# Kernel optimization log

Hardware: AMD Instinct MI355X
Metric: run time of the kernel (lower is better)

Reference implementation:

```python
import jax, jax.numpy as jnp
import numpy as np

IN_DIM = 9
HIDDEN = 32
SORT_K = 30


def setup_inputs() -> dict:
    key = jax.random.key(0)
    ks = jax.random.split(key, 16)
    N, E, G = 250000, 2500000, 2048
    x = jax.random.normal(ks[0], (N, IN_DIM), dtype=jnp.float32)
    edge_index = jax.random.randint(ks[1], (2, E), 0, N, dtype=jnp.int32)
    batch = jnp.sort(jax.random.randint(ks[2], (N,), 0, G, dtype=jnp.int32))
    s = lambda k, sh: jax.random.normal(k, sh, dtype=jnp.float32) * 0.05
    return {
        "x": x, "edge_index": edge_index, "batch": batch, "num_graphs": G,
        "W1": s(ks[3], (IN_DIM, HIDDEN)), "b1": jnp.zeros((HIDDEN,), jnp.float32),
        "W2": s(ks[4], (HIDDEN, HIDDEN)), "b2": jnp.zeros((HIDDEN,), jnp.float32),
        "W3": s(ks[5], (HIDDEN, HIDDEN)), "b3": jnp.zeros((HIDDEN,), jnp.float32),
        "cw1": s(ks[6], (16, HIDDEN, 5)), "cb1": jnp.zeros((16,), jnp.float32),
        "cw2": s(ks[7], (32, 16, 5)), "cb2": jnp.zeros((32,), jnp.float32),
        "lw1": s(ks[8], (32 * (SORT_K - 8), 128)), "lb1": jnp.zeros((128,), jnp.float32),
        "lw2": s(ks[9], (128, 1)), "lb2": jnp.zeros((1,), jnp.float32),
    }


def _gcn(x, W, b, src, dst, dis, n):
    # PyG-style GCNConv: sym-normalized A+I, linear transform first.
    h = x @ W                                     # [N, H]
    msg = h[src] * (dis[src] * dis[dst])[:, None]  # [E, H]
    agg = jax.ops.segment_sum(msg, dst, num_segments=n)
    agg = agg + h * (dis * dis)[:, None]           # self-loops
    return agg + b


def _sort_pool(x, batch, num_graphs, k):
    n, h = x.shape
    key = x[:, -1]
    order = jnp.lexsort((-key, batch))             # by graph, key descending
    xs = x[order]
    bs = batch[order]
    counts = jax.ops.segment_sum(jnp.ones((n,), jnp.int32), batch, num_segments=num_graphs)
    starts = jnp.cumsum(counts) - counts           # exclusive prefix sum
    pos = jnp.arange(n, dtype=jnp.int32) - starts[bs]
    valid = pos < k
    g = jnp.where(valid, bs, num_graphs)           # out-of-range -> dropped
    p = jnp.where(valid, pos, 0)
    out = jnp.zeros((num_graphs, k, h), x.dtype)
    return out.at[g, p].set(xs, mode="drop")


def _conv1d(x, w, b):
    # x: [B, C, T], w: [O, I, K]
    y = jax.lax.conv_general_dilated(x, w, window_strides=(1,), padding="VALID",
                                     dimension_numbers=("NCH", "OIH", "NCH"))
    return y + b[None, :, None]


def reference(x, edge_index, batch, num_graphs, W1, b1, W2, b2, W3, b3,
              cw1, cb1, cw2, cb2, lw1, lb1, lw2, lb2):
    n = x.shape[0]
    src, dst = edge_index[0], edge_index[1]
    deg = jax.ops.segment_sum(jnp.ones_like(src, dtype=x.dtype), dst, num_segments=n) + 1.0
    dis = jax.lax.rsqrt(deg)
    h = jax.nn.relu(_gcn(x, W1, b1, src, dst, dis, n))
    h = jax.nn.relu(_gcn(h, W2, b2, src, dst, dis, n))
    h = jax.nn.relu(_gcn(h, W3, b3, src, dst, dis, n))
    p = _sort_pool(h, batch, num_graphs, SORT_K)   # [G, K, H]
    p = jnp.transpose(p, (0, 2, 1))                # [G, H, K]
    p = jax.nn.relu(_conv1d(p, cw1, cb1))
    p = jax.nn.relu(_conv1d(p, cw2, cb2))
    p = p.reshape(num_graphs, -1)
    p = jax.nn.relu(p @ lw1 + lb1)
    return (p @ lw2 + lb2).reshape(-1)
```

## Files before the change

kernel.cpp:

```cpp
#include <hip/hip_runtime.h>

typedef unsigned long long ull;

#define HIDDEN 32
#define SORTK 30
#define KCAP 256
#define GPB 2
#define BSH 7
#define BNODES (1 << BSH)
#define BCAP 1536
#define HMAX 2048
#define NSEG 256
#define SRC_BITS 18
#define SRC_MASK ((1u << SRC_BITS) - 1)
#define EID_SH  SRC_BITS
#define LD_SH   (SRC_BITS + 22)

static inline int ceil_div_i(long long a, int b){ return (int)((a + b - 1) / b); }

__global__ __launch_bounds__(1024) void hist_kernel(const int* __restrict__ dsts,
                                                    int* __restrict__ hist,
                                                    int E, int NB, int segsz){
  __shared__ int h[HMAX];
  for (int i = threadIdx.x; i < NB; i += 1024) h[i] = 0;
  __syncthreads();
  int seg = blockIdx.x;
  int e0 = seg * segsz;
  int e1 = e0 + segsz; if (e1 > E) e1 = E;
  for (int e = e0 + threadIdx.x; e < e1; e += 1024)
    atomicAdd(&h[dsts[e] >> BSH], 1);
  __syncthreads();
  for (int i = threadIdx.x; i < NB; i += 1024) hist[seg * NB + i] = h[i];
}

__global__ __launch_bounds__(256) void segscanA(const int* __restrict__ hist,
                                                int* __restrict__ segoff,
                                                int* __restrict__ btot,
                                                int NB, int S){
  int wv = (blockIdx.x * 256 + threadIdx.x) >> 6;
  int lane = threadIdx.x & 63;
  if (wv >= NB) return;
  int b = wv;
  int run_base = 0;
  for (int chunk = 0; chunk < S; chunk += 64){
    int s = chunk + lane;
    int v = (s < S) ? hist[(size_t)s * NB + b] : 0;
    int x = v;
    #pragma unroll
    for (int o = 1; o < 64; o <<= 1){ int y = __shfl_up(x, o, 64); if (lane >= o) x += y; }
    if (s < S) segoff[(size_t)s * NB + b] = run_base + x - v;
    run_base += __shfl(x, 63, 64);
  }
  if (lane == 0) btot[b] = run_base;
}

__global__ __launch_bounds__(1024) void segscanB(const int* __restrict__ btot,
                                                 int* __restrict__ bbase, int NB){
  int t = threadIdx.x;
  int b0 = t * 2, b1 = t * 2 + 1;
  int v0 = (b0 < NB) ? btot[b0] : 0;
  int v1 = (b1 < NB) ? btot[b1] : 0;
  int pair = v0 + v1;
  int lane = t & 63, wid = t >> 6;
  int x = pair;
  for (int o = 1; o < 64; o <<= 1){ int y = __shfl_up(x, o, 64); if (lane >= o) x += y; }
  __shared__ int wsum[16]; __shared__ int woff[16];
  if (lane == 63) wsum[wid] = x;
  __syncthreads();
  if (t == 0){ int run = 0; for (int w = 0; w < 16; w++){ woff[w] = run; run += wsum[w]; } }
  __syncthreads();
  int excl = x - pair + woff[wid];
  if (b0 < NB) bbase[b0] = excl;
  if (b1 < NB) bbase[b1] = excl + v0;
}

__global__ __launch_bounds__(1024) void scatter_kernel(const int* __restrict__ dsts,
                                                       const int* __restrict__ srcs,
                                                       const int* __restrict__ segoff,
                                                       const int* __restrict__ bbase,
                                                       ull* __restrict__ staging,
                                                       int E, int NB, int segsz){
  __shared__ int cur[HMAX];
  int seg = blockIdx.x;
  for (int i = threadIdx.x; i < NB; i += 1024) cur[i] = segoff[seg * NB + i] + bbase[i];
  __syncthreads();
  int e0 = seg * segsz;
  int e1 = e0 + segsz; if (e1 > E) e1 = E;
  for (int e = e0 + threadIdx.x; e < e1; e += 1024){
    int d = dsts[e];
    int slot = atomicAdd(&cur[d >> BSH], 1);
    staging[slot] = ((ull)(d & (BNODES - 1)) << LD_SH) | ((ull)e << EID_SH)
                  | (ull)(unsigned)srcs[e];
  }
}

__global__ __launch_bounds__(BNODES) void bucket_sort_kernel(
    const int* __restrict__ bbase, const ull* __restrict__ staging,
    int* __restrict__ csr, int* __restrict__ offs,
    float* __restrict__ dis, int N, int NB, int E){
  __shared__ ull ebuf[BCAP];
  __shared__ ull obuf[BCAP];
  __shared__ int cnt[BNODES];
  __shared__ int cur[BNODES];
  __shared__ int base0[BNODES];
  __shared__ int w0tot;
  int b = blockIdx.x, t = threadIdx.x;
  int n0 = b << BSH;
  int n1 = n0 + BNODES; if (n1 > N) n1 = N;
  int gbeg = bbase[b];
  int gend = (b + 1 < NB) ? bbase[b + 1] : E;
  int cnt_all = gend - gbeg;
  cnt[t] = 0;
  __syncthreads();

  if (cnt_all <= BCAP){
    for (int i = t; i < cnt_all; i += BNODES){
      ull k = staging[gbeg + i];
      ebuf[i] = k;
      atomicAdd(&cnt[(int)(k >> LD_SH)], 1);
    }
    __syncthreads();
    int v = cnt[t];
    int lane = t & 63, wid = t >> 6;
    int x = v;
    for (int o = 1; o < 64; o <<= 1){ int y = __shfl_up(x, o, 64); if (lane >= o) x += y; }
    if (wid == 0 && lane == 63) w0tot = x;
    __syncthreads();
    int ls = x - v + (wid ? w0tot : 0);
    cur[t] = ls;
    base0[t] = ls;
    int n = n0 + t;
    if (n < n1){
      float dd = (float)v + 1.0f;
      dis[n]  = __fdiv_rn(1.0f, __fsqrt_rn(dd));
      offs[n] = gbeg + ls;
    }
    __syncthreads();
    for (int i = t; i < cnt_all; i += BNODES){
      ull k = ebuf[i];
      int pos = atomicAdd(&cur[(int)(k >> LD_SH)], 1);
      obuf[pos] = k;
    }
    __syncthreads();
    for (int i = t; i < cnt_all; i += BNODES){
      ull k = obuf[i];
      int nd = (int)(k >> LD_SH);
      int base = base0[nd];
      int vn = cnt[nd];
      int r = 0;
      for (int j = 0; j < vn; j++) r += (obuf[base + j] < k) ? 1 : 0;
      csr[gbeg + base + r] = (int)(k & SRC_MASK);
    }
  } else {
    int n = n0 + t;
    int deg = 0;
    if (n < n1){
      for (int i = gbeg; i < gend; i++) if ((int)(staging[i] >> LD_SH) == t) deg++;
      float dd = (float)deg + 1.0f;
      dis[n] = __fdiv_rn(1.0f, __fsqrt_rn(dd));
    }
    cnt[t] = (n < n1) ? deg : 0;
    __syncthreads();
    if (n < n1){
      int ls = gbeg; for (int q = 0; q < t; q++) ls += cnt[q];
      offs[n] = ls;
      ull prev = 0;
      for (int o = 0; o < deg; o++){
        ull best = ~0ull;
        for (int i = gbeg; i < gend; i++){
          ull k = staging[i];
          if ((int)(k >> LD_SH) == t && (o == 0 || k > prev) && k < best) best = k;
        }
        csr[ls + o] = (int)(best & SRC_MASK); prev = best;
      }
    }
  }
  if (b == 0 && t == 0) offs[N] = E;
}

template<int K>
__global__ void node_matmul(const float* __restrict__ xin, const float* __restrict__ W,
                            float* __restrict__ H, int N){
  __shared__ float Ws[K * 32];
  for (int i = threadIdx.x; i < K * 32; i += blockDim.x) Ws[i] = W[i];
  __syncthreads();
  int tid = blockIdx.x * blockDim.x + threadIdx.x;
  int n = tid >> 5, c = tid & 31;
  if (n >= N) return;
  const float* xr = xin + (size_t)n * K;
  float acc = 0.f;
  #pragma unroll
  for (int k = 0; k < K; k++) acc = fmaf(xr[k], Ws[k * 32 + c], acc);
  H[(size_t)n * 32 + c] = acc;
}

__device__ __forceinline__ float4 acc_edge(float4 a, float4 h, float w){
  a.x = __fadd_rn(a.x, __fmul_rn(h.x, w));
  a.y = __fadd_rn(a.y, __fmul_rn(h.y, w));
  a.z = __fadd_rn(a.z, __fmul_rn(h.z, w));
  a.w = __fadd_rn(a.w, __fmul_rn(h.w, w));
  return a;
}

__device__ __forceinline__ float4 agg_body(const float* __restrict__ H,
                                           const int* __restrict__ offsets,
                                           const int* __restrict__ csr,
                                           const float* __restrict__ dis,
                                           const float* __restrict__ bias,
                                           int n, int qw){
  const float4* __restrict__ H4 = (const float4*)H;
  float dn = dis[n];
  int s = offsets[n], e = offsets[n + 1];
  float4 acc = make_float4(0.f, 0.f, 0.f, 0.f);
  int i = s;
  for (; i + 8 <= e; i += 8){
    int s0 = csr[i],   s1 = csr[i+1], s2 = csr[i+2], s3 = csr[i+3];
    int s4 = csr[i+4], s5 = csr[i+5], s6 = csr[i+6], s7 = csr[i+7];
    float4 h0 = H4[(size_t)s0 * 8 + qw];
    float4 h1 = H4[(size_t)s1 * 8 + qw];
    float4 h2 = H4[(size_t)s2 * 8 + qw];
    float4 h3 = H4[(size_t)s3 * 8 + qw];
    float4 h4 = H4[(size_t)s4 * 8 + qw];
    float4 h5 = H4[(size_t)s5 * 8 + qw];
    float4 h6 = H4[(size_t)s6 * 8 + qw];
    float4 h7 = H4[(size_t)s7 * 8 + qw];
    float w0 = __fmul_rn(dis[s0], dn), w1 = __fmul_rn(dis[s1], dn);
    float w2 = __fmul_rn(dis[s2], dn), w3 = __fmul_rn(dis[s3], dn);
    float w4 = __fmul_rn(dis[s4], dn), w5 = __fmul_rn(dis[s5], dn);
    float w6 = __fmul_rn(dis[s6], dn), w7 = __fmul_rn(dis[s7], dn);
    acc = acc_edge(acc, h0, w0);
    acc = acc_edge(acc, h1, w1);
    acc = acc_edge(acc, h2, w2);
    acc = acc_edge(acc, h3, w3);
    acc = acc_edge(acc, h4, w4);
    acc = acc_edge(acc, h5, w5);
    acc = acc_edge(acc, h6, w6);
    acc = acc_edge(acc, h7, w7);
  }
  for (; i < e; i++){
    int sr = csr[i];
    float w = __fmul_rn(dis[sr], dn);
    acc = acc_edge(acc, H4[(size_t)sr * 8 + qw], w);
  }
  float4 hn = H4[(size_t)n * 8 + qw];
  float sw = __fmul_rn(dn, dn);
  float4 bb = ((const float4*)bias)[qw];
  float4 v;
  v.x = fmaxf(__fadd_rn(__fadd_rn(acc.x, __fmul_rn(hn.x, sw)), bb.x), 0.f);
  v.y = fmaxf(__fadd_rn(__fadd_rn(acc.y, __fmul_rn(hn.y, sw)), bb.y), 0.f);
  v.z = fmaxf(__fadd_rn(__fadd_rn(acc.z, __fmul_rn(hn.z, sw)), bb.z), 0.f);
  v.w = fmaxf(__fadd_rn(__fadd_rn(acc.w, __fmul_rn(hn.w, sw)), bb.w), 0.f);
  return v;
}

__global__ __launch_bounds__(256) void agg_kernel(const float* __restrict__ H,
                           const int* __restrict__ offsets,
                           const int* __restrict__ csr, const float* __restrict__ dis,
                           const float* __restrict__ bias, float* __restrict__ A,
                           float* __restrict__ keyout, int N){
  int tid = blockIdx.x * 256 + threadIdx.x;
  int n = tid >> 3, qw = tid & 7;
  if (n >= N) return;
  float4 v = agg_body(H, offsets, csr, dis, bias, n, qw);
  ((float4*)A)[(size_t)n * 8 + qw] = v;
  if (keyout != nullptr && qw == 7) keyout[n] = v.w;
}

__global__ __launch_bounds__(256) void agg_mm_kernel(const float* __restrict__ H,
                           const int* __restrict__ offsets,
                           const int* __restrict__ csr, const float* __restrict__ dis,
                           const float* __restrict__ bias,
                           const float* __restrict__ Wn,
                           float* __restrict__ H2, int N){
  int tid = blockIdx.x * 256 + threadIdx.x;
  int n = tid >> 3, qw = tid & 7;
  if (n >= N) return;
  float4 v = agg_body(H, offsets, csr, dis, bias, n, qw);

  const float4* __restrict__ Wn4 = (const float4*)Wn;
  float4 o = make_float4(0.f, 0.f, 0.f, 0.f);
  #pragma unroll
  for (int p = 0; p < 8; p++){
    float4 hp;
    hp.x = __shfl(v.x, p, 8);
    hp.y = __shfl(v.y, p, 8);
    hp.z = __shfl(v.z, p, 8);
    hp.w = __shfl(v.w, p, 8);
    float4 wa = Wn4[(4 * p + 0) * 8 + qw];
    float4 wb = Wn4[(4 * p + 1) * 8 + qw];
    float4 wc = Wn4[(4 * p + 2) * 8 + qw];
    float4 wd = Wn4[(4 * p + 3) * 8 + qw];
    o.x = fmaf(hp.x, wa.x, o.x); o.y = fmaf(hp.x, wa.y, o.y);
    o.z = fmaf(hp.x, wa.z, o.z); o.w = fmaf(hp.x, wa.w, o.w);
    o.x = fmaf(hp.y, wb.x, o.x); o.y = fmaf(hp.y, wb.y, o.y);
    o.z = fmaf(hp.y, wb.z, o.z); o.w = fmaf(hp.y, wb.w, o.w);
    o.x = fmaf(hp.z, wc.x, o.x); o.y = fmaf(hp.z, wc.y, o.y);
    o.z = fmaf(hp.z, wc.z, o.z); o.w = fmaf(hp.z, wc.w, o.w);
    o.x = fmaf(hp.w, wd.x, o.x); o.y = fmaf(hp.w, wd.y, o.y);
    o.z = fmaf(hp.w, wd.z, o.z); o.w = fmaf(hp.w, wd.w, o.w);
  }
  ((float4*)H2)[(size_t)n * 8 + qw] = o;
}

__global__ void gstarts_kernel(const int* __restrict__ batch, int* __restrict__ gstarts,
                               int N, int G){
  int g = blockIdx.x * blockDim.x + threadIdx.x;
  if (g > G) return;
  int lo = 0, hi = N;
  while (lo < hi){ int mid = (lo + hi) >> 1; if (batch[mid] < g) lo = mid + 1; else hi = mid; }
  gstarts[g] = lo;
}

__global__ __launch_bounds__(512) void head_kernel(
    const float* __restrict__ A, const float* __restrict__ keys,
    const int* __restrict__ gstarts,
    const float* __restrict__ cw1, const float* __restrict__ cb1,
    const float* __restrict__ cw2, const float* __restrict__ cb2,
    const float* __restrict__ lw1, const float* __restrict__ lb1,
    const float* __restrict__ lw2, const float* __restrict__ lb2,
    float* __restrict__ out, int G){
  int t = threadIdx.x;
  int sub = t >> 8, lt = t & 255;
  int g = blockIdx.x * GPB + sub;

  __shared__ float w1s[16 * 32 * 5];
  __shared__ float w2s[32 * 16 * 5];
  __shared__ float bufA[GPB][960];
  __shared__ float bufB[GPB][416];
  __shared__ int   sel[GPB][SORTK];

  for (int i = t; i < 2560; i += 512) w1s[i] = cw1[i];
  for (int i = t; i < 2560; i += 512) w2s[i] = cw2[i];
  for (int i = lt; i < 960; i += 256) bufA[sub][i] = 0.f;

  bool valid = (g < G);
  int s = 0, c = 0;
  if (valid){ s = gstarts[g]; c = gstarts[g + 1] - s; }
  bool fast = valid && (c <= KCAP);
  if (fast)
    for (int i = lt; i < c; i += 256) bufB[sub][i] = keys[s + i];
  __syncthreads();

  if (valid){
    if (fast){
      for (int i = lt; i < c; i += 256){
        float ki = bufB[sub][i];
        int rank = 0;
        #pragma unroll 8
        for (int j = 0; j < c; j++){
          float kj = bufB[sub][j];
          rank += (kj > ki || (kj == ki && j < i)) ? 1 : 0;
        }
        if (rank < SORTK) sel[sub][rank] = i;
      }
    } else {
      for (int i = lt; i < c; i += 256){
        float ki = keys[s + i];
        int rank = 0;
        for (int j = 0; j < c; j++){
          float kj = keys[s + j];
          if (kj > ki || (kj == ki && j < i)){
            if (++rank >= SORTK) break;
          }
        }
        if (rank < SORTK) sel[sub][rank] = i;
      }
    }
  }
  __syncthreads();

  if (valid){
    int kk = c < SORTK ? c : SORTK;
    for (int q = lt; q < kk * 32; q += 256){
      int pos = q >> 5, ch = q & 31;
      bufA[sub][ch * 30 + pos] = A[(size_t)(s + sel[sub][pos]) * 32 + ch];
    }
  }
  __syncthreads();

  if (valid){
    for (int q = lt; q < 16 * 26; q += 256){
      int o = q / 26, tt = q - o * 26;
      float acc = cb1[o];
      const float* wo = &w1s[o * 160];
      #pragma unroll 4
      for (int i = 0; i < 32; i++){
        const float* si = &bufA[sub][i * 30 + tt];
        #pragma unroll
        for (int k = 0; k < 5; k++) acc = fmaf(si[k], wo[i * 5 + k], acc);
      }
      bufB[sub][q] = fmaxf(acc, 0.f);
    }
  }
  __syncthreads();

  if (valid){
    for (int q = lt; q < 32 * 22; q += 256){
      int o = q / 22, tt = q - o * 22;
      float acc = cb2[o];
      const float* wo = &w2s[o * 80];
      #pragma unroll 4
      for (int i = 0; i < 16; i++){
        const float* si = &bufB[sub][i * 26 + tt];
        #pragma unroll
        for (int k = 0; k < 5; k++) acc = fmaf(si[k], wo[i * 5 + k], acc);
      }
      bufA[sub][q] = fmaxf(acc, 0.f);
    }
  }
  __syncthreads();

  if (valid){
    int outi = lt & 127, half = lt >> 7;
    float acc = half ? 0.f : lb1[outi];
    const int j0 = half * 352;
    #pragma unroll 8
    for (int j = 0; j < 352; j++){
      int jj = j0 + j;
      acc = fmaf(bufA[sub][jj], lw1[(size_t)jj * 128 + outi], acc);
    }
    bufB[sub][half * 128 + outi] = acc;
  }
  __syncthreads();
  if (valid && lt < 128) bufB[sub][lt] = fmaxf(bufB[sub][lt] + bufB[sub][128 + lt], 0.f);
  __syncthreads();

  if (valid && lt < 64){
    float v = __fadd_rn(__fmul_rn(bufB[sub][lt], lw2[lt]),
                        __fmul_rn(bufB[sub][lt + 64], lw2[lt + 64]));
    #pragma unroll
    for (int o = 32; o > 0; o >>= 1) v += __shfl_xor(v, o, 64);
    if (lt == 0) out[g] = v + lb2[0];
  }
}

extern "C" void kernel_launch(void* const* d_in, const int* in_sizes, int n_in,
                              void* d_out, int out_size, void* d_ws, size_t ws_size,
                              hipStream_t stream){
  const float* x     = (const float*)d_in[0];
  const int*   ei    = (const int*)  d_in[1];
  const int*   batch = (const int*)  d_in[2];
  const float* W1  = (const float*)d_in[4];
  const float* b1  = (const float*)d_in[5];
  const float* W2  = (const float*)d_in[6];
  const float* b2  = (const float*)d_in[7];
  const float* W3  = (const float*)d_in[8];
  const float* b3  = (const float*)d_in[9];
  const float* cw1 = (const float*)d_in[10];
  const float* cb1 = (const float*)d_in[11];
  const float* cw2 = (const float*)d_in[12];
  const float* cb2 = (const float*)d_in[13];
  const float* lw1 = (const float*)d_in[14];
  const float* lb1 = (const float*)d_in[15];
  const float* lw2 = (const float*)d_in[16];
  const float* lb2 = (const float*)d_in[17];

  int N = in_sizes[0] / 9;
  int E = in_sizes[1] / 2;
  int G = out_size;
  const int* srcs = ei;
  const int* dsts = ei + E;
  int NB = ceil_div_i(N, BNODES);
  int segsz = ceil_div_i(E, NSEG);

  char* base = (char*)d_ws;
  size_t off = 0;
  auto alloc = [&](size_t bytes) -> void* {
    off = (off + 255) & ~(size_t)255;
    void* r = base + off; off += bytes; return r;
  };
  float* dis    = (float*)alloc((size_t)N * 4);
  float* H      = (float*)alloc((size_t)N * 32 * 4);
  float* A      = (float*)alloc((size_t)N * 32 * 4);
  float* keyarr = (float*)alloc((size_t)N * 4);
  int*   offs   = (int*)alloc((size_t)(N + 1) * 4);
  int*   csr    = (int*)alloc((size_t)E * 4);
  int*   gst    = (int*)alloc((size_t)(G + 1) * 4);
  int*   hist   = (int*)alloc((size_t)NSEG * NB * 4);
  int*   segoff = (int*)alloc((size_t)NSEG * NB * 4);
  int*   btot   = (int*)alloc((size_t)NB * 4);
  int*   bbase  = (int*)alloc((size_t)(NB + 1) * 4);
  ull*   staging = (ull*)H;
  (void)ws_size; (void)n_in;

  hist_kernel<<<NSEG, 1024, 0, stream>>>(dsts, hist, E, NB, segsz);
  segscanA<<<ceil_div_i(NB * 64, 256), 256, 0, stream>>>(hist, segoff, btot, NB, NSEG);
  segscanB<<<1, 1024, 0, stream>>>(btot, bbase, NB);
  scatter_kernel<<<NSEG, 1024, 0, stream>>>(dsts, srcs, segoff, bbase, staging, E, NB, segsz);
  bucket_sort_kernel<<<NB, BNODES, 0, stream>>>(bbase, staging, csr, offs, dis, N, NB, E);

  int ntm = ceil_div_i((long long)N * 32, 256);
  int nta = ceil_div_i((long long)N * 8, 256);
  node_matmul<9><<<ntm, 256, 0, stream>>>(x, W1, H, N);
  agg_mm_kernel<<<nta, 256, 0, stream>>>(H, offs, csr, dis, b1, W2, A, N);
  agg_mm_kernel<<<nta, 256, 0, stream>>>(A, offs, csr, dis, b2, W3, H, N);
  agg_kernel<<<nta, 256, 0, stream>>>(H, offs, csr, dis, b3, A, keyarr, N);

  gstarts_kernel<<<ceil_div_i(G + 1, 256), 256, 0, stream>>>(batch, gst, N, G);
  head_kernel<<<ceil_div_i(G, GPB), 512, 0, stream>>>(A, keyarr, gst, cw1, cb1, cw2, cb2,
                                                      lw1, lb1, lw2, lb2, (float*)d_out, G);
}
```

Measured before the change: 478.2 us.

## Replace per-segment histogram scan with global atomic bucket reservation in scatter

Drops the per-segment histogram matrix and its column scan kernel. The histogram kernel now atomically accumulates bucket totals directly, and the scatter kernel recomputes a local histogram per block and reserves its output ranges with global atomics on a cursor array. The scatter also moves to more, smaller blocks. This removes one kernel launch and the large hist/segoff traffic, at the cost of reading the destinations twice in scatter and of a nondeterministic order of blocks within each bucket.

```diff
diff --git a/kernel.cpp b/kernel.cpp
--- a/kernel.cpp
+++ b/kernel.cpp
@@ -10,7 +10,8 @@
 #define BNODES (1 << BSH)
 #define BCAP 1536
 #define HMAX 2048
-#define NSEG 256
+#define NSEGH 256
+#define NSEGS 1024
 #define SRC_BITS 18
 #define SRC_MASK ((1u << SRC_BITS) - 1)
 #define EID_SH  SRC_BITS
@@ -19,43 +20,23 @@
 static inline int ceil_div_i(long long a, int b){ return (int)((a + b - 1) / b); }
 
 __global__ __launch_bounds__(1024) void hist_kernel(const int* __restrict__ dsts,
-                                                    int* __restrict__ hist,
+                                                    int* __restrict__ btot,
                                                     int E, int NB, int segsz){
   __shared__ int h[HMAX];
   for (int i = threadIdx.x; i < NB; i += 1024) h[i] = 0;
   __syncthreads();
-  int seg = blockIdx.x;
-  int e0 = seg * segsz;
+  int e0 = blockIdx.x * segsz;
   int e1 = e0 + segsz; if (e1 > E) e1 = E;
   for (int e = e0 + threadIdx.x; e < e1; e += 1024)
     atomicAdd(&h[dsts[e] >> BSH], 1);
   __syncthreads();
-  for (int i = threadIdx.x; i < NB; i += 1024) hist[seg * NB + i] = h[i];
-}
-
-__global__ __launch_bounds__(256) void segscanA(const int* __restrict__ hist,
-                                                int* __restrict__ segoff,
-                                                int* __restrict__ btot,
-                                                int NB, int S){
-  int wv = (blockIdx.x * 256 + threadIdx.x) >> 6;
-  int lane = threadIdx.x & 63;
-  if (wv >= NB) return;
-  int b = wv;
-  int run_base = 0;
-  for (int chunk = 0; chunk < S; chunk += 64){
-    int s = chunk + lane;
-    int v = (s < S) ? hist[(size_t)s * NB + b] : 0;
-    int x = v;
-    #pragma unroll
-    for (int o = 1; o < 64; o <<= 1){ int y = __shfl_up(x, o, 64); if (lane >= o) x += y; }
-    if (s < S) segoff[(size_t)s * NB + b] = run_base + x - v;
-    run_base += __shfl(x, 63, 64);
-  }
-  if (lane == 0) btot[b] = run_base;
+  for (int i = threadIdx.x; i < NB; i += 1024)
+    if (h[i]) atomicAdd(&btot[i], h[i]);
 }
 
 __global__ __launch_bounds__(1024) void segscanB(const int* __restrict__ btot,
-                                                 int* __restrict__ bbase, int NB){
+                                                 int* __restrict__ bbase,
+                                                 int* __restrict__ gcur, int NB){
   int t = threadIdx.x;
   int b0 = t * 2, b1 = t * 2 + 1;
   int v0 = (b0 < NB) ? btot[b0] : 0;
@@ -70,27 +51,36 @@
   if (t == 0){ int run = 0; for (int w = 0; w < 16; w++){ woff[w] = run; run += wsum[w]; } }
   __syncthreads();
   int excl = x - pair + woff[wid];
-  if (b0 < NB) bbase[b0] = excl;
-  if (b1 < NB) bbase[b1] = excl + v0;
-}
-
-__global__ __launch_bounds__(1024) void scatter_kernel(const int* __restrict__ dsts,
-                                                       const int* __restrict__ srcs,
-                                                       const int* __restrict__ segoff,
-                                                       const int* __restrict__ bbase,
-                                                       ull* __restrict__ staging,
-                                                       int E, int NB, int segsz){
-  __shared__ int cur[HMAX];
-  int seg = blockIdx.x;
-  for (int i = threadIdx.x; i < NB; i += 1024) cur[i] = segoff[seg * NB + i] + bbase[i];
-  __syncthreads();
-  int e0 = seg * segsz;
+  if (b0 < NB){ bbase[b0] = excl;      gcur[b0] = excl; }
+  if (b1 < NB){ bbase[b1] = excl + v0; gcur[b1] = excl + v0; }
+}
+
+__global__ __launch_bounds__(512) void scatter_kernel(const int* __restrict__ dsts,
+                                                      const int* __restrict__ srcs,
+                                                      int* __restrict__ gcur,
+                                                      ull* __restrict__ staging,
+                                                      int E, int NB, int segsz){
+  __shared__ int lh[HMAX];
+  __shared__ int lbase[HMAX];
+  for (int i = threadIdx.x; i < NB; i += 512) lh[i] = 0;
+  __syncthreads();
+  int e0 = blockIdx.x * segsz;
   int e1 = e0 + segsz; if (e1 > E) e1 = E;
-  for (int e = e0 + threadIdx.x; e < e1; e += 1024){
+  for (int e = e0 + threadIdx.x; e < e1; e += 512)
+    atomicAdd(&lh[dsts[e] >> BSH], 1);
+  __syncthreads();
+  for (int b = threadIdx.x; b < NB; b += 512){
+    int c = lh[b];
+    lbase[b] = c ? atomicAdd(&gcur[b], c) : 0;
+    lh[b] = 0;
+  }
+  __syncthreads();
+  for (int e = e0 + threadIdx.x; e < e1; e += 512){
     int d = dsts[e];
-    int slot = atomicAdd(&cur[d >> BSH], 1);
-    staging[slot] = ((ull)(d & (BNODES - 1)) << LD_SH) | ((ull)e << EID_SH)
-                  | (ull)(unsigned)srcs[e];
+    int bk = d >> BSH;
+    int idx = atomicAdd(&lh[bk], 1);
+    staging[lbase[bk] + idx] = ((ull)(d & (BNODES - 1)) << LD_SH) | ((ull)e << EID_SH)
+                             | (ull)(unsigned)srcs[e];
   }
 }
 
@@ -461,7 +451,8 @@
   const int* srcs = ei;
   const int* dsts = ei + E;
   int NB = ceil_div_i(N, BNODES);
-  int segsz = ceil_div_i(E, NSEG);
+  int segszH = ceil_div_i(E, NSEGH);
+  int segszS = ceil_div_i(E, NSEGS);
 
   char* base = (char*)d_ws;
   size_t off = 0;
@@ -476,17 +467,16 @@
   int*   offs   = (int*)alloc((size_t)(N + 1) * 4);
   int*   csr    = (int*)alloc((size_t)E * 4);
   int*   gst    = (int*)alloc((size_t)(G + 1) * 4);
-  int*   hist   = (int*)alloc((size_t)NSEG * NB * 4);
-  int*   segoff = (int*)alloc((size_t)NSEG * NB * 4);
   int*   btot   = (int*)alloc((size_t)NB * 4);
   int*   bbase  = (int*)alloc((size_t)(NB + 1) * 4);
+  int*   gcur   = (int*)alloc((size_t)NB * 4);
   ull*   staging = (ull*)H;
   (void)ws_size; (void)n_in;
 
-  hist_kernel<<<NSEG, 1024, 0, stream>>>(dsts, hist, E, NB, segsz);
-  segscanA<<<ceil_div_i(NB * 64, 256), 256, 0, stream>>>(hist, segoff, btot, NB, NSEG);
-  segscanB<<<1, 1024, 0, stream>>>(btot, bbase, NB);
-  scatter_kernel<<<NSEG, 1024, 0, stream>>>(dsts, srcs, segoff, bbase, staging, E, NB, segsz);
+  hipMemsetAsync(btot, 0, (size_t)NB * 4, stream);
+  hist_kernel<<<NSEGH, 1024, 0, stream>>>(dsts, btot, E, NB, segszH);
+  segscanB<<<1, 1024, 0, stream>>>(btot, bbase, gcur, NB);
+  scatter_kernel<<<NSEGS, 512, 0, stream>>>(dsts, srcs, gcur, staging, E, NB, segszS);
   bucket_sort_kernel<<<NB, BNODES, 0, stream>>>(bbase, staging, csr, offs, dis, N, NB, E);
 
   int ntm = ceil_div_i((long long)N * 32, 256);
```

Result: slower. 518.8 us (+8.5%).
